# Performance work log

Measured on AMD Instinct MI355X. Metric: run time of the kernel, lower is better.

## Reference

```python
import jax, jax.numpy as jnp
import numpy as np
from jax import lax

N, C_IN, H, W = 32, 128, 64, 64
C_OUT, KH, KW = 256, 3, 3
C_DIM = 64


def setup_inputs() -> dict:
    key = jax.random.key(0)
    k1, k2, k3, k4, k5 = jax.random.split(key, 5)
    return {
        "x": jax.random.normal(k1, (N, C_IN, H, W), dtype=jnp.float32),
        "c": jax.random.normal(k2, (N, C_DIM), dtype=jnp.float32),
        "weight": jax.random.normal(k3, (C_OUT, C_IN, KH, KW), dtype=jnp.float32),
        "c_weight": jax.random.normal(k4, (C_OUT, C_DIM), dtype=jnp.float32),
        "bias": jax.random.normal(k5, (C_OUT,), dtype=jnp.float32),
    }


def reference(x, c, weight, c_weight, bias):
    # Equivalent to the module's unfold + matmul path (groups=1, dilation=1,
    # zero padding=1, stride=1): a direct conv fused with the spatially
    # invariant context bias c @ c_weight^T and the channel bias.
    out = lax.conv_general_dilated(
        x, weight,
        window_strides=(1, 1),
        padding=((1, 1), (1, 1)),
        dimension_numbers=("NCHW", "OIHW", "NCHW"),
    )  # (N, C_out, H, W)
    ctx = jnp.einsum("nd,od->no", c, c_weight)  # (N, C_out), same at every spatial loc
    return out + ctx[:, :, None, None] + bias[None, :, None, None]
```

## Files before the change

### kernel.cpp

```cpp
#include <hip/hip_runtime.h>
#include <hip/hip_bf16.h>


#define NN   32
#define CIN  128
#define HH   64
#define WW   64
#define COUT 256
#define CDIM 64
#define HP   66
#define WP   66

#define XP_BYTES  ((size_t)NN*HP*WP*CIN*2)
#define WT_BYTES  ((size_t)9*COUT*CIN*2)
#define CTX_BYTES ((size_t)NN*COUT*4)
#define WS_NEEDED (XP_BYTES + WT_BYTES + CTX_BYTES)

typedef __attribute__((ext_vector_type(8))) short short8;
typedef __attribute__((ext_vector_type(4))) float float4v;

__device__ __forceinline__ void async16(const void* g, void* l) {
    __builtin_amdgcn_global_load_lds(
        (const __attribute__((address_space(1))) unsigned int*)g,
        (__attribute__((address_space(3))) unsigned int*)l, 16, 0, 0);
}

#define SETPRIO(x) __builtin_amdgcn_s_setprio(x)

__global__ __launch_bounds__(256) void prep_all(
    const float* __restrict__ x, const float* __restrict__ c,
    const float* __restrict__ wgt, const float* __restrict__ cw,
    const float* __restrict__ bias,
    __hip_bfloat16* __restrict__ xP, __hip_bfloat16* __restrict__ wT,
    float* __restrict__ ctx)
{
    __shared__ float tile[CIN][65];
    int bid = blockIdx.x;
    int t   = threadIdx.x;

    if (bid < 2048) {
        int n = bid >> 6;
        int h = bid & 63;
        const float* xb = x + (size_t)n * CIN * HH * WW + (size_t)h * WW;

        int lane16 = t & 15, rgrp = t >> 4;
        #pragma unroll
        for (int i = 0; i < 8; ++i) {
            int ci = rgrp + i * 16;
            float4v v = *(const float4v*)(xb + (size_t)ci * (HH * WW) + lane16 * 4);
            int w0 = lane16 * 4;
            tile[ci][w0]     = v.x;
            tile[ci][w0 + 1] = v.y;
            tile[ci][w0 + 2] = v.z;
            tile[ci][w0 + 3] = v.w;
        }
        __syncthreads();

        int oct = t & 3, w = t >> 2;
        __hip_bfloat16* db = xP + (((size_t)n * HP + (h + 1)) * WP + (w + 1)) * CIN;
        #pragma unroll
        for (int p = 0; p < 4; ++p) {
            int ci0 = p * 32 + oct * 8;
            union { short8 v; __hip_bfloat16 b[8]; } u;
            #pragma unroll
            for (int j = 0; j < 8; ++j)
                u.b[j] = __float2bfloat16(tile[ci0 + j][w]);
            *(short8*)(db + ci0) = u.v;
        }
    } else if (bid < 2568) {
        int g = (bid - 2048) * 256 + t;
        int n   = g / 4160;
        int rem = g - n * 4160;
        int pi  = rem >> 4;
        int oct = rem & 15;
        int hh, ww;
        if (pi < 132) { hh = (pi >= 66) ? 65 : 0; ww = pi % 66; }
        else { int p2 = pi - 132; ww = (p2 >= 64) ? 65 : 0; hh = 1 + (p2 & 63); }
        short8 z = {};
        *(short8*)(xP + (((size_t)n * HP + hh) * WP + ww) * CIN + oct * 8) = z;
    } else {
        int b2 = bid - 2568;
        if (b2 < 1152) {
            int idx = b2 * 256 + t;
            int ci  = idx & 127;
            int co  = (idx >> 7) & 255;
            int tap = idx >> 15;
            wT[idx] = __float2bfloat16(wgt[((size_t)co * CIN + ci) * 9 + tap]);
        } else {
            int idx = (b2 - 1152) * 256 + t;
            int co = idx & 255, n = idx >> 8;
            float a = bias[co];
            #pragma unroll 8
            for (int d = 0; d < CDIM; ++d) a += c[n * CDIM + d] * cw[co * CDIM + d];
            ctx[idx] = a;
        }
    }
}

__global__ __launch_bounds__(512, 2) void conv_mfma(
    const __hip_bfloat16* __restrict__ xP,
    const __hip_bfloat16* __restrict__ wT,
    const float* __restrict__ ctx,
    float* __restrict__ out)
{
    __shared__ __align__(16) short A_s[50688];

    int bid = blockIdx.x;
    int mt  = (bid & 7) * 64 + (bid >> 3);
    int n   = mt >> 4;
    int h0  = (mt & 15) << 2;

    int tid  = threadIdx.x;
    int lane = tid & 63, wv = tid >> 6;
    int wm = (wv & 1) * 128;
    int wn = (wv >> 1) * 64;
    int l15 = lane & 15, lu = lane >> 4;

    const __hip_bfloat16* xPn = xP + (size_t)(n * HP + h0) * WP * CIN;
    #pragma unroll
    for (int rnd = 0; rnd < 13; ++rnd) {
        int g = rnd * 512 + tid;
        if (g < 6336) {
            int r  = g >> 4, cc = g & 15;
            int hh = r / 66;
            int ww = r - hh * 66;
            int so = ((cc & 7) ^ (r & 7)) | (cc & 8);
            async16(xPn + ((size_t)hh * WP + ww) * CIN + so * 8, &A_s[g * 8]);
        }
    }

    const __hip_bfloat16* wB = wT + ((size_t)(wn + l15) * CIN) + lu * 8;

    short8 bCur[4], bNxt[4];
    #pragma unroll
    for (int ni = 0; ni < 4; ++ni)
        bCur[ni] = *(const short8*)(wB + (size_t)ni * (16 * CIN));

    __syncthreads();

    int ohc = wm >> 6;
    float4v acc[8][4] = {};

    for (int tap = 0; tap < 9; ++tap) {
        int kh  = (tap * 11) >> 5, kw = tap - kh * 3;
        int rb0 = (ohc + kh) * 66 + l15 + kw;
        #pragma unroll
        for (int kb = 0; kb < 4; ++kb) {
            int s1 = tap * 4 + kb + 1;
            if (s1 > 35) s1 = 0;
            int tap1 = s1 >> 2, kb1 = s1 & 3;
            const __hip_bfloat16* wNx = wB + (size_t)tap1 * (COUT * CIN) + kb1 * 32;
            #pragma unroll
            for (int ni = 0; ni < 4; ++ni)
                bNxt[ni] = *(const short8*)(wNx + (size_t)ni * (16 * CIN));

            int cL = kb * 4 + lu;
            int c7 = cL & 7;
            int cg = (cL & 8) << 3;
            short8 aF[8];
            #pragma unroll
            for (int mi = 0; mi < 8; ++mi) {
                int r    = rb0 + (mi >> 2) * 66 + (mi & 3) * 16;
                int phys = c7 ^ (r & 7);
                aF[mi] = *(const short8*)&A_s[r * 128 + cg + phys * 8];
            }

            SETPRIO(1);
            #pragma unroll
            for (int mi = 0; mi < 8; ++mi)
                #pragma unroll
                for (int ni = 0; ni < 4; ++ni)
                    acc[mi][ni] = __builtin_amdgcn_mfma_f32_16x16x32_bf16(
                        aF[mi], bCur[ni], acc[mi][ni], 0, 0, 0);
            SETPRIO(0);

            #pragma unroll
            for (int ni = 0; ni < 4; ++ni) bCur[ni] = bNxt[ni];
        }
    }

    #pragma unroll
    for (int ni = 0; ni < 4; ++ni) {
        int co = wn + ni * 16 + l15;
        float cv = ctx[n * COUT + co];
        float* ob = out + ((size_t)n * COUT + co) * (HH * WW);
        #pragma unroll
        for (int mi = 0; mi < 8; ++mi) {
            int rp = wm + mi * 16 + (lu << 2);
            int hh = h0 + (rp >> 6);
            int ww = rp & 63;
            float4v v = acc[mi][ni] + cv;
            *(float4v*)&ob[hh * WW + ww] = v;
        }
    }
}

__global__ __launch_bounds__(256) void contextual_conv_f32(
    const float* __restrict__ x, const float* __restrict__ c,
    const float* __restrict__ wgt, const float* __restrict__ cw,
    const float* __restrict__ bias, float* __restrict__ out)
{
    int idx = blockIdx.x * 256 + threadIdx.x;
    int w = idx & 63, h = (idx >> 6) & 63, cb = (idx >> 12) & 63, n = idx >> 18;
    float acc[4];
    #pragma unroll
    for (int j = 0; j < 4; ++j) acc[j] = bias[cb + j * 64];
    const float* cp = c + n * CDIM;
    for (int d = 0; d < CDIM; ++d) {
        float cv = cp[d];
        #pragma unroll
        for (int j = 0; j < 4; ++j) acc[j] += cv * cw[(cb + j * 64) * CDIM + d];
    }
    const float* xn = x + (size_t)n * (CIN * HH * WW);
    for (int ci = 0; ci < CIN; ++ci) {
        const float* xc = xn + ci * (HH * WW);
        float wv[4][9];
        #pragma unroll
        for (int j = 0; j < 4; ++j) {
            const float* wp = wgt + ((cb + j * 64) * CIN + ci) * 9;
            #pragma unroll
            for (int k = 0; k < 9; ++k) wv[j][k] = wp[k];
        }
        #pragma unroll
        for (int kh = 0; kh < 3; ++kh) {
            int hh = h + kh - 1;
            if (hh < 0 || hh >= HH) continue;
            const float* xr = xc + hh * WW;
            #pragma unroll
            for (int kw = 0; kw < 3; ++kw) {
                int ww = w + kw - 1;
                if (ww < 0 || ww >= WW) continue;
                float xv = xr[ww];
                #pragma unroll
                for (int j = 0; j < 4; ++j) acc[j] += xv * wv[j][kh * 3 + kw];
            }
        }
    }
    size_t obase = (size_t)n * (COUT * HH * WW) + (size_t)h * WW + w;
    #pragma unroll
    for (int j = 0; j < 4; ++j)
        out[obase + (size_t)(cb + j * 64) * (HH * WW)] = acc[j];
}

extern "C" void kernel_launch(void* const* d_in, const int* in_sizes, int n_in,
                              void* d_out, int out_size, void* d_ws, size_t ws_size,
                              hipStream_t stream) {
    const float* x    = (const float*)d_in[0];
    const float* c    = (const float*)d_in[1];
    const float* wgt  = (const float*)d_in[2];
    const float* cw   = (const float*)d_in[3];
    const float* bias = (const float*)d_in[4];
    float* out = (float*)d_out;

    if (ws_size < WS_NEEDED) {
        const int total_threads = NN * 64 * HH * WW;
        contextual_conv_f32<<<total_threads / 256, 256, 0, stream>>>(x, c, wgt, cw, bias, out);
        return;
    }

    char* ws = (char*)d_ws;
    __hip_bfloat16* xP = (__hip_bfloat16*)ws;
    __hip_bfloat16* wT = (__hip_bfloat16*)(ws + XP_BYTES);
    float*          cx = (float*)(ws + XP_BYTES + WT_BYTES);

    prep_all <<<3752, 256, 0, stream>>>(x, c, wgt, cw, bias, xP, wT, cx);
    conv_mfma<<<512, 512, 0, stream>>>(xP, wT, cx, out);
}
```

Measured before the change: 270.6 us.

## Fuse input transpose and padding into conv kernel, halve tile height

Drops the separate pass that wrote a padded NHWC bf16 copy of x. The conv kernel now reads fp32 NCHW x directly, converts it to bf16 and writes it into an LDS tile with a zero-filled halo. The tile shrinks to 2 output rows (1024 blocks, launch bounds raised to 4 per CU), and the XOR swizzle is replaced by a padded row stride. This removes a full round trip of the input through global memory, at the cost of strided 4-byte global loads, synchronous staging with no async copy, and less weight reuse per block.

Result: slower. 317.7 us (+17.4%).

```diff
diff --git a/kernel.cpp b/kernel.cpp
--- a/kernel.cpp
+++ b/kernel.cpp
@@ -8,127 +8,62 @@
 #define WW   64
 #define COUT 256
 #define CDIM 64
-#define HP   66
-#define WP   66
-
-#define XP_BYTES  ((size_t)NN*HP*WP*CIN*2)
+
 #define WT_BYTES  ((size_t)9*COUT*CIN*2)
 #define CTX_BYTES ((size_t)NN*COUT*4)
-#define WS_NEEDED (XP_BYTES + WT_BYTES + CTX_BYTES)
+#define WS_NEEDED (WT_BYTES + CTX_BYTES)
+
+#define AROWS 264
+#define ARSTR 136
+#define ACHNK 4488
 
 typedef __attribute__((ext_vector_type(8))) short short8;
 typedef __attribute__((ext_vector_type(4))) float float4v;
 
-__device__ __forceinline__ void async16(const void* g, void* l) {
-    __builtin_amdgcn_global_load_lds(
-        (const __attribute__((address_space(1))) unsigned int*)g,
-        (__attribute__((address_space(3))) unsigned int*)l, 16, 0, 0);
-}
-
 #define SETPRIO(x) __builtin_amdgcn_s_setprio(x)
 
-__global__ __launch_bounds__(256) void prep_all(
-    const float* __restrict__ x, const float* __restrict__ c,
-    const float* __restrict__ wgt, const float* __restrict__ cw,
-    const float* __restrict__ bias,
-    __hip_bfloat16* __restrict__ xP, __hip_bfloat16* __restrict__ wT,
-    float* __restrict__ ctx)
-{
-    __shared__ float tile[CIN][65];
+__global__ __launch_bounds__(256) void prep_wc(const float* __restrict__ wgt,
+                                               const float* __restrict__ c,
+                                               const float* __restrict__ cw,
+                                               const float* __restrict__ bias,
+                                               __hip_bfloat16* __restrict__ wT,
+                                               float* __restrict__ ctx) {
     int bid = blockIdx.x;
-    int t   = threadIdx.x;
-
-    if (bid < 2048) {
-        int n = bid >> 6;
-        int h = bid & 63;
-        const float* xb = x + (size_t)n * CIN * HH * WW + (size_t)h * WW;
-
-        int lane16 = t & 15, rgrp = t >> 4;
-        #pragma unroll
-        for (int i = 0; i < 8; ++i) {
-            int ci = rgrp + i * 16;
-            float4v v = *(const float4v*)(xb + (size_t)ci * (HH * WW) + lane16 * 4);
-            int w0 = lane16 * 4;
-            tile[ci][w0]     = v.x;
-            tile[ci][w0 + 1] = v.y;
-            tile[ci][w0 + 2] = v.z;
-            tile[ci][w0 + 3] = v.w;
-        }
-        __syncthreads();
-
-        int oct = t & 3, w = t >> 2;
-        __hip_bfloat16* db = xP + (((size_t)n * HP + (h + 1)) * WP + (w + 1)) * CIN;
-        #pragma unroll
-        for (int p = 0; p < 4; ++p) {
-            int ci0 = p * 32 + oct * 8;
-            union { short8 v; __hip_bfloat16 b[8]; } u;
-            #pragma unroll
-            for (int j = 0; j < 8; ++j)
-                u.b[j] = __float2bfloat16(tile[ci0 + j][w]);
-            *(short8*)(db + ci0) = u.v;
-        }
-    } else if (bid < 2568) {
-        int g = (bid - 2048) * 256 + t;
-        int n   = g / 4160;
-        int rem = g - n * 4160;
-        int pi  = rem >> 4;
-        int oct = rem & 15;
-        int hh, ww;
-        if (pi < 132) { hh = (pi >= 66) ? 65 : 0; ww = pi % 66; }
-        else { int p2 = pi - 132; ww = (p2 >= 64) ? 65 : 0; hh = 1 + (p2 & 63); }
-        short8 z = {};
-        *(short8*)(xP + (((size_t)n * HP + hh) * WP + ww) * CIN + oct * 8) = z;
+    if (bid < 1152) {
+        int idx = bid * 256 + threadIdx.x;
+        int ci  = idx & 127;
+        int co  = (idx >> 7) & 255;
+        int tap = idx >> 15;
+        wT[idx] = __float2bfloat16(wgt[((size_t)co * CIN + ci) * 9 + tap]);
     } else {
-        int b2 = bid - 2568;
-        if (b2 < 1152) {
-            int idx = b2 * 256 + t;
-            int ci  = idx & 127;
-            int co  = (idx >> 7) & 255;
-            int tap = idx >> 15;
-            wT[idx] = __float2bfloat16(wgt[((size_t)co * CIN + ci) * 9 + tap]);
-        } else {
-            int idx = (b2 - 1152) * 256 + t;
-            int co = idx & 255, n = idx >> 8;
-            float a = bias[co];
-            #pragma unroll 8
-            for (int d = 0; d < CDIM; ++d) a += c[n * CDIM + d] * cw[co * CDIM + d];
-            ctx[idx] = a;
-        }
-    }
-}
-
-__global__ __launch_bounds__(512, 2) void conv_mfma(
-    const __hip_bfloat16* __restrict__ xP,
+        int idx = (bid - 1152) * 256 + threadIdx.x;
+        int co = idx & 255, n = idx >> 8;
+        float a = bias[co];
+        #pragma unroll 8
+        for (int d = 0; d < CDIM; ++d) a += c[n * CDIM + d] * cw[co * CDIM + d];
+        ctx[idx] = a;
+    }
+}
+
+__global__ __launch_bounds__(512, 4) void conv_mfma(
+    const float* __restrict__ x,
     const __hip_bfloat16* __restrict__ wT,
     const float* __restrict__ ctx,
     float* __restrict__ out)
 {
-    __shared__ __align__(16) short A_s[50688];
+    __shared__ __align__(16) short A_s[AROWS * ARSTR];
 
     int bid = blockIdx.x;
-    int mt  = (bid & 7) * 64 + (bid >> 3);
-    int n   = mt >> 4;
-    int h0  = (mt & 15) << 2;
+    int mt  = (bid & 7) * 128 + (bid >> 3);
+    int n   = mt >> 5;
+    int h0  = (mt & 31) << 1;
 
     int tid  = threadIdx.x;
     int lane = tid & 63, wv = tid >> 6;
-    int wm = (wv & 1) * 128;
+    int wm = (wv & 1) * 64;
     int wn = (wv >> 1) * 64;
     int l15 = lane & 15, lu = lane >> 4;
 
-    const __hip_bfloat16* xPn = xP + (size_t)(n * HP + h0) * WP * CIN;
-    #pragma unroll
-    for (int rnd = 0; rnd < 13; ++rnd) {
-        int g = rnd * 512 + tid;
-        if (g < 6336) {
-            int r  = g >> 4, cc = g & 15;
-            int hh = r / 66;
-            int ww = r - hh * 66;
-            int so = ((cc & 7) ^ (r & 7)) | (cc & 8);
-            async16(xPn + ((size_t)hh * WP + ww) * CIN + so * 8, &A_s[g * 8]);
-        }
-    }
-
     const __hip_bfloat16* wB = wT + ((size_t)(wn + l15) * CIN) + lu * 8;
 
     short8 bCur[4], bNxt[4];
@@ -136,10 +71,34 @@
     for (int ni = 0; ni < 4; ++ni)
         bCur[ni] = *(const short8*)(wB + (size_t)ni * (16 * CIN));
 
+    #pragma unroll
+    for (int z = 0; z < 9; ++z) {
+        int g = z * 512 + tid;
+        if (g < ACHNK) *(short8*)&A_s[g * 8] = (short8){};
+    }
     __syncthreads();
 
+    int h0m1 = h0 - 1;
+    #pragma unroll
+    for (int i = 0; i < 8; ++i) {
+        int task = wv * 8 + i;
+        int hl   = task >> 4;
+        int oct  = task & 15;
+        int hh   = h0m1 + hl;
+        if (hh >= 0 && hh < HH) {
+            const float* src = x + (((size_t)(n * CIN + oct * 8)) * HH + hh) * WW + lane;
+            union { short8 s; __hip_bfloat16 b[8]; } u;
+            #pragma unroll
+            for (int k = 0; k < 8; ++k)
+                u.b[k] = __float2bfloat16(src[(size_t)k * HH * WW]);
+            int row = hl * 66 + 1 + lane;
+            *(short8*)&A_s[row * ARSTR + ((oct) << 3) + 0] = u.s;
+        }
+    }
+    __syncthreads();
+
+    float4v acc[4][4] = {};
     int ohc = wm >> 6;
-    float4v acc[8][4] = {};
 
     for (int tap = 0; tap < 9; ++tap) {
         int kh  = (tap * 11) >> 5, kw = tap - kh * 3;
@@ -155,19 +114,16 @@
                 bNxt[ni] = *(const short8*)(wNx + (size_t)ni * (16 * CIN));
 
             int cL = kb * 4 + lu;
-            int c7 = cL & 7;
-            int cg = (cL & 8) << 3;
-            short8 aF[8];
-            #pragma unroll
-            for (int mi = 0; mi < 8; ++mi) {
-                int r    = rb0 + (mi >> 2) * 66 + (mi & 3) * 16;
-                int phys = c7 ^ (r & 7);
-                aF[mi] = *(const short8*)&A_s[r * 128 + cg + phys * 8];
+            short8 aF[4];
+            #pragma unroll
+            for (int mi = 0; mi < 4; ++mi) {
+                int r = rb0 + mi * 16;
+                aF[mi] = *(const short8*)&A_s[r * ARSTR + cL * 8];
             }
 
             SETPRIO(1);
             #pragma unroll
-            for (int mi = 0; mi < 8; ++mi)
+            for (int mi = 0; mi < 4; ++mi)
                 #pragma unroll
                 for (int ni = 0; ni < 4; ++ni)
                     acc[mi][ni] = __builtin_amdgcn_mfma_f32_16x16x32_bf16(
@@ -185,7 +141,7 @@
         float cv = ctx[n * COUT + co];
         float* ob = out + ((size_t)n * COUT + co) * (HH * WW);
         #pragma unroll
-        for (int mi = 0; mi < 8; ++mi) {
+        for (int mi = 0; mi < 4; ++mi) {
             int rp = wm + mi * 16 + (lu << 2);
             int hh = h0 + (rp >> 6);
             int ww = rp & 63;
@@ -259,10 +215,9 @@
     }
 
     char* ws = (char*)d_ws;
-    __hip_bfloat16* xP = (__hip_bfloat16*)ws;
-    __hip_bfloat16* wT = (__hip_bfloat16*)(ws + XP_BYTES);
-    float*          cx = (float*)(ws + XP_BYTES + WT_BYTES);
-
-    prep_all <<<3752, 256, 0, stream>>>(x, c, wgt, cw, bias, xP, wT, cx);
-    conv_mfma<<<512, 512, 0, stream>>>(xP, wT, cx, out);
-}
+    __hip_bfloat16* wT = (__hip_bfloat16*)ws;
+    float*          cx = (float*)(ws + WT_BYTES);
+
+    prep_wc  <<<1184, 256, 0, stream>>>(wgt, c, cw, bias, wT, cx);
+    conv_mfma<<<1024, 512, 0, stream>>>(x, wT, cx, out);
+}
```
